# Kernel tuning notes

Measured on AMD Instinct MI355X. Metric: run time of the kernel, lower is better.

## Reference

```python
import jax, jax.numpy as jnp
import numpy as np

B, G, C = 32, 50, 80
IMG = 640
STRIDES = (8, 16, 32)
CENTER_RADIUS = 2.5


def _make_grids():
    xs, ys, ss = [], [], []
    for s in STRIDES:
        n = IMG // s
        yv, xv = np.meshgrid(np.arange(n, dtype=np.float32), np.arange(n, dtype=np.float32), indexing='ij')
        xs.append(xv.reshape(-1)); ys.append(yv.reshape(-1))
        ss.append(np.full(n * n, s, dtype=np.float32))
    return np.concatenate(xs), np.concatenate(ys), np.concatenate(ss)


def setup_inputs():
    xg, yg, sg = _make_grids()
    A = xg.shape[0]  # 8400
    ks = jax.random.split(jax.random.key(0), 5)
    # decoded box predictions near grid centers (cxcywh, pixel units)
    ctr = jnp.stack([jnp.asarray((xg + 0.5) * sg), jnp.asarray((yg + 0.5) * sg)], -1)[None] \
        + jax.random.normal(ks[0], (B, A, 2)) * 8.0
    wh = jnp.exp(jax.random.normal(ks[1], (B, A, 2)) * 0.5) * jnp.asarray(sg)[None, :, None] * 4.0
    pred_output = jnp.concatenate([ctr, wh, jax.random.normal(ks[2], (B, A, 1 + C))], -1)  # [B,A,85]
    obj_preds = jax.random.normal(ks[3], (B, A, 1))
    cls_preds = jax.random.normal(ks[4], (B, A, C))
    # labels [B,G,5] = (class, cx, cy, w, h); first num_gt rows valid, rest zero
    rng = np.random.RandomState(0)
    lab = np.zeros((B, G, 5), np.float32)
    for b in range(B):
        ng = rng.randint(5, G)
        lab[b, :ng, 0] = rng.randint(0, C, ng)
        lab[b, :ng, 1:3] = rng.uniform(40.0, IMG - 40.0, (ng, 2))
        lab[b, :ng, 3:5] = rng.uniform(20.0, 160.0, (ng, 2))
    return {"pred_output": pred_output, "obj_preds": obj_preds, "cls_preds": cls_preds,
            "labels": jnp.asarray(lab), "x_shifts": jnp.asarray(xg),
            "y_shifts": jnp.asarray(yg), "strides": jnp.asarray(sg)}


def _pairwise_iou_cxcywh(a, b):
    # a [G,4], b [A,4] -> [G,A]
    tl = jnp.maximum(a[:, None, :2] - a[:, None, 2:] * 0.5, b[None, :, :2] - b[None, :, 2:] * 0.5)
    br = jnp.minimum(a[:, None, :2] + a[:, None, 2:] * 0.5, b[None, :, :2] + b[None, :, 2:] * 0.5)
    area_a = a[:, 2] * a[:, 3]
    area_b = b[:, 2] * b[:, 3]
    en = jnp.all(tl < br, -1).astype(a.dtype)
    area_i = jnp.prod(br - tl, -1) * en
    return area_i / (area_a[:, None] + area_b[None, :] - area_i + 1e-16)


def _assign_one(gt, gt_valid, boxes, cls_logit, obj_logit, xg, yg, sg):
    # SimOTA assignment for a single image, fully vectorized over [G,A].
    # gt [G,5], gt_valid [G], boxes [A,4], cls_logit [A,C], obj_logit [A,1]
    num_gt = gt.shape[0]
    gt_cls = gt[:, 0].astype(jnp.int32)
    gb = gt[:, 1:5]
    xc = (xg + 0.5) * sg
    yc = (yg + 0.5) * sg
    d_box = jnp.stack([
        xc[None, :] - (gb[:, 0:1] - gb[:, 2:3] * 0.5),
        (gb[:, 0:1] + gb[:, 2:3] * 0.5) - xc[None, :],
        yc[None, :] - (gb[:, 1:2] - gb[:, 3:4] * 0.5),
        (gb[:, 1:2] + gb[:, 3:4] * 0.5) - yc[None, :]], -1)
    in_boxes = (jnp.min(d_box, -1) > 0) & gt_valid[:, None]
    d_ctr = jnp.stack([
        xc[None, :] - (gb[:, 0:1] - CENTER_RADIUS * sg[None, :]),
        (gb[:, 0:1] + CENTER_RADIUS * sg[None, :]) - xc[None, :],
        yc[None, :] - (gb[:, 1:2] - CENTER_RADIUS * sg[None, :]),
        (gb[:, 1:2] + CENTER_RADIUS * sg[None, :]) - yc[None, :]], -1)
    in_ctr = (jnp.min(d_ctr, -1) > 0) & gt_valid[:, None]
    fg0 = jnp.any(in_boxes | in_ctr, 0)           # [A] candidate anchors (fg_mask)
    and_ctr = in_boxes & in_ctr                    # [G,A]
    ious = _pairwise_iou_cxcywh(gb, boxes) * fg0[None, :].astype(boxes.dtype) * gt_valid[:, None].astype(boxes.dtype)
    # pairwise BCE(sqrt(sig(cls)*sig(obj)), one_hot) summed over classes, without [G,A,C]
    logq = 0.5 * (jax.nn.log_sigmoid(cls_logit) + jax.nn.log_sigmoid(obj_logit))  # [A,C]
    q = jnp.clip(jnp.exp(logq), 1e-7, 1.0 - 1e-7)
    s_neg = jnp.sum(jnp.log1p(-q), -1)             # [A] sum_c log(1-q_c)
    q_gt = q[:, gt_cls].T                          # [G,A]
    cls_cost = -jnp.log(q_gt) + jnp.log1p(-q_gt) - s_neg[None, :]
    invalid = (~fg0)[None, :] | (~gt_valid)[:, None]
    cost = cls_cost - 3.0 * jnp.log(ious + 1e-8) + 1e5 * (~and_ctr) + 1e9 * invalid
    # dynamic-k: sum of top-10 ious per gt, truncated, min 1
    dyn_k = jnp.maximum(jnp.sum(jax.lax.top_k(ious, 10)[0], -1).astype(jnp.int32), 1)  # [G]
    ranks = jnp.argsort(jnp.argsort(cost, 1), 1)   # rank of each anchor in ascending cost
    matching = (ranks < dyn_k[:, None]) & gt_valid[:, None]
    # resolve anchors claimed by >1 gt: keep min-cost gt
    best_gt = jnp.argmin(cost, 0)                  # [A]
    onehot_best = jnp.arange(num_gt)[:, None] == best_gt[None, :]
    matching = jnp.where(jnp.sum(matching, 0)[None, :] > 1, onehot_best, matching)
    fg = jnp.any(matching, 0)                      # [A] final fg mask
    matched = jnp.argmax(matching, 0)              # [A] matched gt index
    pred_iou = jnp.sum(matching * ious, 0)         # [A]
    cls_t = jax.nn.one_hot(gt_cls[matched], cls_logit.shape[-1], dtype=boxes.dtype) \
        * (pred_iou * fg.astype(boxes.dtype))[:, None]
    return cls_t, fg, matched


def _forward(pred_output, obj_preds, cls_preds, labels, x_shifts, y_shifts, strides):
    bbox = pred_output[:, :, :4]
    gt_valid = labels.sum(-1) > 0
    cls_t, fg, matched = jax.vmap(_assign_one, in_axes=(0, 0, 0, 0, 0, None, None, None))(
        labels, gt_valid, bbox, cls_preds, obj_preds, x_shifts, y_shifts, strides)
    cls_t = jax.lax.stop_gradient(cls_t)  # get_assignments is @torch.no_grad()
    reg_t = jnp.take_along_axis(labels[:, :, 1:5], matched[:, :, None], axis=1)  # [B,A,4]
    fg_f = fg.astype(pred_output.dtype)
    num_fg = jnp.maximum(jnp.sum(fg_f), 1.0)
    # IoU loss (cxcywh), loss = 1 - iou^2, only on fg anchors
    tl = jnp.maximum(bbox[..., :2] - bbox[..., 2:] * 0.5, reg_t[..., :2] - reg_t[..., 2:] * 0.5)
    br = jnp.minimum(bbox[..., :2] + bbox[..., 2:] * 0.5, reg_t[..., :2] + reg_t[..., 2:] * 0.5)
    en = jnp.all(tl < br, -1).astype(bbox.dtype)
    area_i = jnp.prod(br - tl, -1) * en
    area_u = bbox[..., 2] * bbox[..., 3] + reg_t[..., 2] * reg_t[..., 3] - area_i
    iou = area_i / (area_u + 1e-16)
    loss_iou = jnp.sum((1.0 - iou ** 2) * fg_f) / num_fg
    bce = lambda x, y: jax.nn.softplus(x) - x * y  # BCEWithLogits, reduction='none'
    loss_obj = jnp.sum(bce(obj_preds[..., 0], fg_f)) / num_fg
    loss_cls = jnp.sum(bce(cls_preds, cls_t) * fg_f[..., None]) / num_fg
    return 5.0 * loss_iou + loss_obj + loss_cls


def reference(pred_output, obj_preds, cls_preds, labels, x_shifts, y_shifts, strides):
    return _forward(pred_output, obj_preds, cls_preds, labels, x_shifts, y_shifts, strides)
```

## Files before the change

kernel.cpp:

```cpp
#include <hip/hip_runtime.h>
#include <cstdint>
#include <cstddef>

#define BB 32
#define GG 50
#define CC 80
#define AA 8400
#define PCH (5 + CC)
#define NLB ((BB * AA + 255) / 256)
#define FGBIT 63
#define SENTC 3.3e38f
#define SENTI 0x7fffffff

__device__ __forceinline__ float logsig_fast(float x) {
    float e = __expf(-fabsf(x));
    return fminf(x, 0.f) - __logf(1.f + e);
}
__device__ __forceinline__ float softplusf(float x) {
    return fmaxf(x, 0.f) + log1pf(expf(-fabsf(x)));
}

__device__ __forceinline__ float pair_iou(float px, float py, float pw, float ph,
                                          float gx, float gy, float gw, float gh) {
    float tlx = fmaxf(gx - gw * 0.5f, px - pw * 0.5f);
    float tly = fmaxf(gy - gh * 0.5f, py - ph * 0.5f);
    float brx = fminf(gx + gw * 0.5f, px + pw * 0.5f);
    float bry = fminf(gy + gh * 0.5f, py + ph * 0.5f);
    float en = (tlx < brx && tly < bry) ? 1.f : 0.f;
    float ai = (brx - tlx) * (bry - tly) * en;
    return ai / (gw * gh + pw * ph - ai + 1e-16f);
}
__device__ __forceinline__ float cost_val(float x , float lo ,
                                          float sn , float v ,
                                          bool ac, bool f0, bool valid) {
    float lq = 0.5f * (logsig_fast(x) + lo);
    float q = fminf(fmaxf(__expf(lq), 1e-7f), 1.f - 1e-7f);
    float cst = -__logf(q) + __logf(1.f - q) - sn;
    cst -= 3.0f * __logf(v + 1e-8f);
    cst += 100000.0f * (ac ? 0.f : 1.f);
    cst += 1000000000.0f * ((!f0 || !valid) ? 1.f : 0.f);
    return cst;
}

__global__ __launch_bounds__(256)
void k_precompute(const float* __restrict__ pred, const float* __restrict__ obj,
                  const float* __restrict__ cls,
                  float2* __restrict__ lsn, float* __restrict__ sps,
                  float4* __restrict__ pbox) {
    int t = blockIdx.x * blockDim.x + threadIdx.x;
    int i = t >> 2;
    int sub = t & 3;
    if (i >= BB * AA) return;
    float lo = logsig_fast(obj[i]);
    float K = __expf(0.5f * lo);
    const float4* c4 = (const float4*)(cls + (size_t)i * CC);
    float smax = 0.f, psp = 1.f, p1 = 1.f, p2 = 1.f;
#pragma unroll
    for (int j = 0; j < 5; j++) {
        float4 v = c4[sub + 4 * j];
        float xs4[4] = {v.x, v.y, v.z, v.w};
        float pg = 1.f;
#pragma unroll
        for (int u = 0; u < 4; u++) {
            float x = xs4[u];
            float th = __expf(-0.5f * fabsf(x));
            float t2 = th * th;
            smax += fmaxf(x, 0.f);
            psp *= (1.f + t2);
            float qq = K * (x < 0.f ? th : 1.f) * rsqrtf(1.f + t2);
            qq = fminf(fmaxf(qq, 1e-7f), 1.f - 1e-7f);
            pg *= (1.f - qq);
        }
        if (j < 2) p1 *= pg; else p2 *= pg;
    }
    float sp = smax + __logf(psp);
    float sn = __logf(p1) + __logf(p2);
    sp += __shfl_xor(sp, 1); sn += __shfl_xor(sn, 1);
    sp += __shfl_xor(sp, 2); sn += __shfl_xor(sn, 2);
    float pv = pred[(size_t)i * PCH + sub];
    ((float*)pbox)[(size_t)i * 4 + sub] = pv;
    if (sub == 0) {
        lsn[i] = make_float2(lo, sn);
        sps[i] = sp;
    }
}

__global__ void k_geom(const float* __restrict__ labels, const float* __restrict__ xs,
                       const float* __restrict__ ys, const float* __restrict__ ss,
                       unsigned long long* __restrict__ amask,
                       int* __restrict__ clist, int* __restrict__ ccnt) {
    int b = blockIdx.y;
    int a = blockIdx.x * blockDim.x + threadIdx.x;
    __shared__ float lab[GG * 5];
    __shared__ int lv[GG];
    for (int t = threadIdx.x; t < GG * 5; t += blockDim.x) lab[t] = labels[b * GG * 5 + t];
    __syncthreads();
    if (threadIdx.x < GG) {
        const float* r = lab + threadIdx.x * 5;
        lv[threadIdx.x] = ((r[0] + r[1] + r[2] + r[3] + r[4]) > 0.f) ? 1 : 0;
    }
    __syncthreads();
    if (a >= AA) return;
    float s = ss[a];
    float xc = (xs[a] + 0.5f) * s;
    float yc = (ys[a] + 0.5f) * s;
    unsigned long long m = 0;
    int any = 0;
    for (int g = 0; g < GG; g++) {
        if (!lv[g]) continue;
        const float* r = lab + g * 5;
        float gx = r[1], gy = r[2], gw = r[3], gh = r[4];
        float d1 = xc - (gx - gw * 0.5f);
        float d2 = (gx + gw * 0.5f) - xc;
        float d3 = yc - (gy - gh * 0.5f);
        float d4 = (gy + gh * 0.5f) - yc;
        bool ib = fminf(fminf(d1, d2), fminf(d3, d4)) > 0.f;
        float cr = 2.5f * s;
        float e1 = xc - (gx - cr);
        float e2 = (gx + cr) - xc;
        float e3 = yc - (gy - cr);
        float e4 = (gy + cr) - yc;
        bool ic = fminf(fminf(e1, e2), fminf(e3, e4)) > 0.f;
        if (ib || ic) any = 1;
        if (ib && ic) m |= 1ull << g;
    }
    if (any) m |= 1ull << FGBIT;
    amask[b * AA + a] = m;
    int lane = threadIdx.x & 63;
    unsigned long long act = __ballot(m != 0);
    if (act) {
        int leader = __ffsll(act) - 1;
        int base = 0;
        if (lane == leader) base = atomicAdd(&ccnt[b], __popcll(act));
        base = __shfl(base, leader);
        if (m != 0) {
            int off = __popcll(act & ((1ull << lane) - 1ull));
            clist[b * AA + base + off] = a;
        }
    }
}

__global__ __launch_bounds__(256, 4)
void k_assign(const float4* __restrict__ pbox, const float2* __restrict__ lsn,
              const float* __restrict__ cls,
              const unsigned long long* __restrict__ amask,
              const float* __restrict__ labels,
              const int* __restrict__ clist, const int* __restrict__ ccnt,
              unsigned long long* __restrict__ mmask) {
    int w = blockIdx.x;
    int b = w / GG, g = w % GG;
    const float* r = labels + (size_t)w * 5;
    float gcls = r[0], gx = r[1], gy = r[2], gw = r[3], gh = r[4];
    if (!((gcls + gx + gy + gw + gh) > 0.f)) return;
    int gtc = (int)gcls;
    int tid = threadIdx.x;
    int lane = tid & 63;
    int wv = tid >> 6;
    int cnt = ccnt[b];

    float ivl[10];
    float cvl[10];
    int   cil[10];
#pragma unroll
    for (int t = 0; t < 10; t++) { ivl[t] = 0.f; cvl[t] = SENTC; cil[t] = SENTI; }
    int nac = 0;

    for (int i0 = wv * 64; i0 < cnt; i0 += 256) {
        int i = i0 + lane;
        bool inr = i < cnt;
        int a = clist[b * AA + (inr ? i : (cnt - 1))];
        int ia = b * AA + a;
        unsigned long long am = amask[ia];
        float4 pb = pbox[ia];
        bool f0 = inr && ((am >> FGBIT) & 1ull);
        bool ac = inr && ((am >> g) & 1ull);
        nac += __popcll(__ballot(ac));
        float v = f0 ? pair_iou(pb.x, pb.y, pb.z, pb.w, gx, gy, gw, gh) : 0.f;
        {
            float mv = v;
            while (true) {
                unsigned long long mb = __ballot(mv > ivl[9]);
                if (!mb) break;
                int src = __ffsll(mb) - 1;
                float bv = __shfl(mv, src);
#pragma unroll
                for (int t = 0; t < 10; t++)
                    if (bv > ivl[t]) { float tmp = ivl[t]; ivl[t] = bv; bv = tmp; }
                if (lane == src) mv = -1.f;
            }
        }
        {
            float c = SENTC; int id = SENTI;
            if (ac) {
                float x = cls[(size_t)ia * CC + gtc];
                float2 ls = lsn[ia];
                c = cost_val(x, ls.x, ls.y, v, true, true, true);
                id = a;
            }
            while (true) {
                bool enter = (c < cvl[9]) || (c == cvl[9] && id < cil[9]);
                unsigned long long mb = __ballot(enter);
                if (!mb) break;
                int src = __ffsll(mb) - 1;
                float bc = __shfl(c, src);
                int bi = __shfl(id, src);
#pragma unroll
                for (int t = 0; t < 10; t++) {
                    bool sw = (bc < cvl[t]) || (bc == cvl[t] && bi < cil[t]);
                    if (sw) {
                        float tf = cvl[t]; cvl[t] = bc; bc = tf;
                        int ti = cil[t]; cil[t] = bi; bi = ti;
                    }
                }
                if (lane == src) { c = SENTC; id = SENTI; }
            }
        }
    }

    __shared__ float IV[4][10];
    __shared__ float CV[4][10];
    __shared__ int CI[4][10];
    __shared__ int NAC[4];
    __shared__ int s_k, s_n0;
    __shared__ int sel[10];

    if (lane == 0) {
#pragma unroll
        for (int t = 0; t < 10; t++) { IV[wv][t] = ivl[t]; CV[wv][t] = cvl[t]; CI[wv][t] = cil[t]; }
        NAC[wv] = nac;
    }
    __syncthreads();
    if (tid == 0) {
        int h[4] = {0, 0, 0, 0};
        float ssum = 0.f;
        for (int j = 0; j < 10; j++) {
            float bv = -1.f; int bc = 0;
#pragma unroll
            for (int c2 = 0; c2 < 4; c2++)
                if (h[c2] < 10 && IV[c2][h[c2]] > bv) { bv = IV[c2][h[c2]]; bc = c2; }
            ssum += bv;
            h[bc]++;
        }
        int k = (int)ssum;
        if (k < 1) k = 1;
        s_k = k;
        s_n0 = NAC[0] + NAC[1] + NAC[2] + NAC[3];
    }
    __syncthreads();
    int k = s_k;

    if (s_n0 < k) {
        const int chunk = AA / 4;
        int abase = wv * chunk, aend = abase + chunk;
#pragma unroll
        for (int t = 0; t < 10; t++) { cvl[t] = SENTC; cil[t] = SENTI; }
        for (int a0 = abase; a0 < aend; a0 += 64) {
            int a = a0 + lane;
            bool inr = a < aend;
            int ia = b * AA + (inr ? a : (aend - 1));
            unsigned long long am = amask[ia];
            bool f0 = inr && ((am >> FGBIT) & 1ull);
            bool ac = inr && ((am >> g) & 1ull);
            float v = 0.f;
            if (f0) {
                float4 pb = pbox[ia];
                v = pair_iou(pb.x, pb.y, pb.z, pb.w, gx, gy, gw, gh);
            }
            float c = SENTC; int id = SENTI;
            if (inr) {
                float x = cls[(size_t)ia * CC + gtc];
                float2 ls = lsn[ia];
                c = cost_val(x, ls.x, ls.y, v, ac, f0, true);
                id = a;
            }
            while (true) {
                bool enter = (c < cvl[9]) || (c == cvl[9] && id < cil[9]);
                unsigned long long mb = __ballot(enter);
                if (!mb) break;
                int src = __ffsll(mb) - 1;
                float bc = __shfl(c, src);
                int bi = __shfl(id, src);
#pragma unroll
                for (int t = 0; t < 10; t++) {
                    bool sw = (bc < cvl[t]) || (bc == cvl[t] && bi < cil[t]);
                    if (sw) {
                        float tf = cvl[t]; cvl[t] = bc; bc = tf;
                        int ti = cil[t]; cil[t] = bi; bi = ti;
                    }
                }
                if (lane == src) { c = SENTC; id = SENTI; }
            }
        }
        if (lane == 0) {
#pragma unroll
            for (int t = 0; t < 10; t++) { CV[wv][t] = cvl[t]; CI[wv][t] = cil[t]; }
        }
        __syncthreads();
    }

    if (tid == 0) {
        int h[4] = {0, 0, 0, 0};
        for (int j = 0; j < k; j++) {
            float bv = SENTC; int bix = SENTI; int bc = 0;
#pragma unroll
            for (int c2 = 0; c2 < 4; c2++) {
                if (h[c2] < 10) {
                    float av = CV[c2][h[c2]]; int ax = CI[c2][h[c2]];
                    if (av < bv || (av == bv && ax < bix)) { bv = av; bix = ax; bc = c2; }
                }
            }
            sel[j] = bix;
            h[bc]++;
        }
    }
    __syncthreads();
    if (tid < k) {
        atomicOr(&mmask[(size_t)b * AA + sel[tid]], 1ull << g);
    }
}

__global__ void k_loss(const float4* __restrict__ pbox, const float* __restrict__ obj,
                       const float* __restrict__ cls, const float* __restrict__ labels,
                       const float2* __restrict__ lsn,
                       const unsigned long long* __restrict__ amask,
                       const unsigned long long* __restrict__ mmask,
                       const float* __restrict__ sps, float* __restrict__ partial) {
    int i = blockIdx.x * blockDim.x + threadIdx.x;
    float li = 0.f, lo = 0.f, lc = 0.f, nf = 0.f;
    if (i < BB * AA) {
        int b = i / AA, a = i % AA;
        unsigned long long m = mmask[i];
        int cnt = __popcll(m);
        bool fg = (m != 0);
        int mg = 0;
        float4 pb = pbox[i];
        unsigned long long am = amask[i];
        bool f0 = (am >> FGBIT) & 1ull;
        if (cnt > 1) {
            float2 ls = lsn[i];
            float bv = 3.4e38f;
            for (int g = 0; g < GG; g++) {
                const float* r = labels + (size_t)(b * GG + g) * 5;
                float gcls = r[0], gx = r[1], gy = r[2], gw = r[3], gh = r[4];
                bool valid = (gcls + gx + gy + gw + gh) > 0.f;
                int gtc = (int)gcls;
                float raw = pair_iou(pb.x, pb.y, pb.z, pb.w, gx, gy, gw, gh);
                float v = raw * (f0 ? 1.f : 0.f) * (valid ? 1.f : 0.f);
                float x = cls[(size_t)i * CC + gtc];
                bool ac = (am >> g) & 1ull;
                float cst = cost_val(x, ls.x, ls.y, v, ac, f0, valid);
                if (cst < bv) { bv = cst; mg = g; }
            }
        } else if (cnt == 1) {
            mg = __ffsll((unsigned long long)m) - 1;
        }
        float o = obj[i];
        lo = softplusf(o) - (fg ? o : 0.f);
        if (fg) {
            const float* r = labels + (size_t)(b * GG + mg) * 5;
            float gcls = r[0], gx = r[1], gy = r[2], gw = r[3], gh = r[4];
            bool valid = (gcls + gx + gy + gw + gh) > 0.f;
            int gtc = (int)gcls;
            float piou = pair_iou(pb.x, pb.y, pb.z, pb.w, gx, gy, gw, gh)
                         * (f0 ? 1.f : 0.f) * (valid ? 1.f : 0.f);
            float tlx = fmaxf(pb.x - pb.z * 0.5f, gx - gw * 0.5f);
            float tly = fmaxf(pb.y - pb.w * 0.5f, gy - gh * 0.5f);
            float brx = fminf(pb.x + pb.z * 0.5f, gx + gw * 0.5f);
            float bry = fminf(pb.y + pb.w * 0.5f, gy + gh * 0.5f);
            float en = (tlx < brx && tly < bry) ? 1.f : 0.f;
            float ai = (brx - tlx) * (bry - tly) * en;
            float u = pb.z * pb.w + gw * gh - ai;
            float v2 = ai / (u + 1e-16f);
            li = 1.f - v2 * v2;
            lc = sps[i] - cls[(size_t)i * CC + gtc] * piou;
            nf = 1.f;
        }
    }
    for (int off = 32; off; off >>= 1) {
        li += __shfl_down(li, off);
        lo += __shfl_down(lo, off);
        lc += __shfl_down(lc, off);
        nf += __shfl_down(nf, off);
    }
    __shared__ float red[4][4];
    int wid = threadIdx.x >> 6;
    if ((threadIdx.x & 63) == 0) {
        red[wid][0] = li; red[wid][1] = lo; red[wid][2] = lc; red[wid][3] = nf;
    }
    __syncthreads();
    if (threadIdx.x == 0) {
        float s0 = 0.f, s1 = 0.f, s2 = 0.f, s3 = 0.f;
#pragma unroll
        for (int t = 0; t < 4; t++) {
            s0 += red[t][0]; s1 += red[t][1]; s2 += red[t][2]; s3 += red[t][3];
        }
        float4* pb = (float4*)partial;
        pb[blockIdx.x] = make_float4(s0, s1, s2, s3);
    }
}

__global__ void k_final(const float* __restrict__ partial, float* __restrict__ out) {
    int tid = threadIdx.x;
    float s0 = 0.f, s1 = 0.f, s2 = 0.f, s3 = 0.f;
    const float4* pb = (const float4*)partial;
    for (int i = tid; i < NLB; i += 256) {
        float4 v = pb[i];
        s0 += v.x; s1 += v.y; s2 += v.z; s3 += v.w;
    }
    for (int off = 32; off; off >>= 1) {
        s0 += __shfl_down(s0, off);
        s1 += __shfl_down(s1, off);
        s2 += __shfl_down(s2, off);
        s3 += __shfl_down(s3, off);
    }
    __shared__ float red[4][4];
    int wid = tid >> 6;
    if ((tid & 63) == 0) {
        red[wid][0] = s0; red[wid][1] = s1; red[wid][2] = s2; red[wid][3] = s3;
    }
    __syncthreads();
    if (tid == 0) {
        float li = 0.f, lo = 0.f, lc = 0.f, nf = 0.f;
#pragma unroll
        for (int t = 0; t < 4; t++) {
            li += red[t][0]; lo += red[t][1]; lc += red[t][2]; nf += red[t][3];
        }
        nf = fmaxf(nf, 1.f);
        out[0] = (5.f * li + lo + lc) / nf;
    }
}

extern "C" void kernel_launch(void* const* d_in, const int* in_sizes, int n_in,
                              void* d_out, int out_size, void* d_ws, size_t ws_size,
                              hipStream_t stream) {
    const float* pred = (const float*)d_in[0];
    const float* obj  = (const float*)d_in[1];
    const float* cls  = (const float*)d_in[2];
    const float* lab  = (const float*)d_in[3];
    const float* xs   = (const float*)d_in[4];
    const float* ys   = (const float*)d_in[5];
    const float* ss   = (const float*)d_in[6];
    float* out = (float*)d_out;

    const size_t BA = (size_t)BB * AA;

    float2* lsn  = (float2*)d_ws;
    float*  sps  = (float*)(lsn + BA);
    float4* pbox = (float4*)(sps + BA);
    unsigned long long* amask = (unsigned long long*)(pbox + BA);
    unsigned long long* mmask = amask + BA;
    float* partial = (float*)(mmask + BA);
    int* clist = (int*)(partial + (size_t)NLB * 4);
    int* ccnt  = clist + BA;

    hipMemsetAsync(mmask, 0, BA * sizeof(unsigned long long), stream);
    hipMemsetAsync(ccnt, 0, BB * sizeof(int), stream);

    dim3 blk(256);
    k_precompute<<<dim3((BB * AA * 4 + 255) / 256), blk, 0, stream>>>(pred, obj, cls,
                                                                      lsn, sps, pbox);
    k_geom<<<dim3((AA + 255) / 256, BB), blk, 0, stream>>>(lab, xs, ys, ss, amask,
                                                           clist, ccnt);
    k_assign<<<dim3(BB * GG), blk, 0, stream>>>(pbox, lsn, cls, amask, lab,
                                                clist, ccnt, mmask);
    k_loss<<<dim3(NLB), blk, 0, stream>>>(pbox, obj, cls, lab, lsn, amask,
                                          mmask, sps, partial);
    k_final<<<1, blk, 0, stream>>>(partial, out);
}
```

Baseline: 170.6 us.

## Use per-lane top-10 lists with butterfly merge instead of serialized ballot insertion

The per-GT top-k selection used to keep one wave-wide top-10 list, inserting candidates one lane at a time through a ballot/shuffle loop. Now each lane keeps its own private top-10 lists for IoU and cost. At the end, 10 rounds of xor-shuffle argmax/argmin reductions extract the wave's top 10. This removes the serialized insertion loops when many lanes qualify, at the cost of more registers and a fixed reduction cost.

```diff
diff --git a/kernel.cpp b/kernel.cpp
--- a/kernel.cpp
+++ b/kernel.cpp
@@ -163,56 +163,36 @@
     int   cil[10];
 #pragma unroll
     for (int t = 0; t < 10; t++) { ivl[t] = 0.f; cvl[t] = SENTC; cil[t] = SENTI; }
-    int nac = 0;
-
-    for (int i0 = wv * 64; i0 < cnt; i0 += 256) {
-        int i = i0 + lane;
-        bool inr = i < cnt;
-        int a = clist[b * AA + (inr ? i : (cnt - 1))];
+    int nlc = 0;
+
+    for (int i0 = wv * 64 + lane; i0 < cnt; i0 += 256) {
+        int a = clist[b * AA + i0];
         int ia = b * AA + a;
         unsigned long long am = amask[ia];
         float4 pb = pbox[ia];
-        bool f0 = inr && ((am >> FGBIT) & 1ull);
-        bool ac = inr && ((am >> g) & 1ull);
-        nac += __popcll(__ballot(ac));
+        bool f0 = (am >> FGBIT) & 1ull;
+        bool ac = (am >> g) & 1ull;
+        nlc += ac ? 1 : 0;
         float v = f0 ? pair_iou(pb.x, pb.y, pb.z, pb.w, gx, gy, gw, gh) : 0.f;
-        {
+        if (v > ivl[9]) {
             float mv = v;
-            while (true) {
-                unsigned long long mb = __ballot(mv > ivl[9]);
-                if (!mb) break;
-                int src = __ffsll(mb) - 1;
-                float bv = __shfl(mv, src);
-#pragma unroll
-                for (int t = 0; t < 10; t++)
-                    if (bv > ivl[t]) { float tmp = ivl[t]; ivl[t] = bv; bv = tmp; }
-                if (lane == src) mv = -1.f;
-            }
-        }
-        {
-            float c = SENTC; int id = SENTI;
-            if (ac) {
-                float x = cls[(size_t)ia * CC + gtc];
-                float2 ls = lsn[ia];
-                c = cost_val(x, ls.x, ls.y, v, true, true, true);
-                id = a;
-            }
-            while (true) {
-                bool enter = (c < cvl[9]) || (c == cvl[9] && id < cil[9]);
-                unsigned long long mb = __ballot(enter);
-                if (!mb) break;
-                int src = __ffsll(mb) - 1;
-                float bc = __shfl(c, src);
-                int bi = __shfl(id, src);
+#pragma unroll
+            for (int t = 0; t < 10; t++)
+                if (mv > ivl[t]) { float tmp = ivl[t]; ivl[t] = mv; mv = tmp; }
+        }
+        if (ac) {
+            float2 ls = lsn[ia];
+            float c = cost_val(cls[(size_t)ia * CC + gtc], ls.x, ls.y, v, true, true, true);
+            int id = a;
+            if (c < cvl[9] || (c == cvl[9] && id < cil[9])) {
 #pragma unroll
                 for (int t = 0; t < 10; t++) {
-                    bool sw = (bc < cvl[t]) || (bc == cvl[t] && bi < cil[t]);
+                    bool sw = (c < cvl[t]) || (c == cvl[t] && id < cil[t]);
                     if (sw) {
-                        float tf = cvl[t]; cvl[t] = bc; bc = tf;
-                        int ti = cil[t]; cil[t] = bi; bi = ti;
+                        float tf = cvl[t]; cvl[t] = c; c = tf;
+                        int ti = cil[t]; cil[t] = id; id = ti;
                     }
                 }
-                if (lane == src) { c = SENTC; id = SENTI; }
             }
         }
     }
@@ -224,12 +204,51 @@
     __shared__ int s_k, s_n0;
     __shared__ int sel[10];
 
-    if (lane == 0) {
-#pragma unroll
-        for (int t = 0; t < 10; t++) { IV[wv][t] = ivl[t]; CV[wv][t] = cvl[t]; CI[wv][t] = cil[t]; }
-        NAC[wv] = nac;
-    }
-    __syncthreads();
+    {
+        int s = nlc;
+#pragma unroll
+        for (int off = 1; off < 64; off <<= 1) s += __shfl_xor(s, off);
+        if (lane == 0) NAC[wv] = s;
+    }
+
+    for (int rr = 0; rr < 10; rr++) {
+        float bv = ivl[0];
+        int bl = lane;
+#pragma unroll
+        for (int off = 1; off < 64; off <<= 1) {
+            float ov = __shfl_xor(bv, off);
+            int ol = __shfl_xor(bl, off);
+            if (ov > bv || (ov == bv && ol < bl)) { bv = ov; bl = ol; }
+        }
+        if (lane == 0) IV[wv][rr] = bv;
+        if (lane == bl) {
+#pragma unroll
+            for (int t = 0; t < 9; t++) ivl[t] = ivl[t + 1];
+            ivl[9] = 0.f;
+        }
+    }
+
+    for (int rr = 0; rr < 10; rr++) {
+        float bc = cvl[0];
+        int bi = cil[0];
+        int bl = lane;
+#pragma unroll
+        for (int off = 1; off < 64; off <<= 1) {
+            float oc = __shfl_xor(bc, off);
+            int oi = __shfl_xor(bi, off);
+            int ol = __shfl_xor(bl, off);
+            bool tk = (oc < bc) || (oc == bc && (oi < bi || (oi == bi && ol < bl)));
+            if (tk) { bc = oc; bi = oi; bl = ol; }
+        }
+        if (lane == 0) { CV[wv][rr] = bc; CI[wv][rr] = bi; }
+        if (lane == bl) {
+#pragma unroll
+            for (int t = 0; t < 9; t++) { cvl[t] = cvl[t + 1]; cil[t] = cil[t + 1]; }
+            cvl[9] = SENTC; cil[9] = SENTI;
+        }
+    }
+    __syncthreads();
+
     if (tid == 0) {
         int h[4] = {0, 0, 0, 0};
         float ssum = 0.f;
@@ -250,10 +269,10 @@
     int k = s_k;
 
     if (s_n0 < k) {
+#pragma unroll
+        for (int t = 0; t < 10; t++) { cvl[t] = SENTC; cil[t] = SENTI; }
         const int chunk = AA / 4;
         int abase = wv * chunk, aend = abase + chunk;
-#pragma unroll
-        for (int t = 0; t < 10; t++) { cvl[t] = SENTC; cil[t] = SENTI; }
         for (int a0 = abase; a0 < aend; a0 += 64) {
             int a = a0 + lane;
             bool inr = a < aend;
@@ -273,27 +292,35 @@
                 c = cost_val(x, ls.x, ls.y, v, ac, f0, true);
                 id = a;
             }
-            while (true) {
-                bool enter = (c < cvl[9]) || (c == cvl[9] && id < cil[9]);
-                unsigned long long mb = __ballot(enter);
-                if (!mb) break;
-                int src = __ffsll(mb) - 1;
-                float bc = __shfl(c, src);
-                int bi = __shfl(id, src);
+            if (c < cvl[9] || (c == cvl[9] && id < cil[9])) {
 #pragma unroll
                 for (int t = 0; t < 10; t++) {
-                    bool sw = (bc < cvl[t]) || (bc == cvl[t] && bi < cil[t]);
+                    bool sw = (c < cvl[t]) || (c == cvl[t] && id < cil[t]);
                     if (sw) {
-                        float tf = cvl[t]; cvl[t] = bc; bc = tf;
-                        int ti = cil[t]; cil[t] = bi; bi = ti;
+                        float tf = cvl[t]; cvl[t] = c; c = tf;
+                        int ti = cil[t]; cil[t] = id; id = ti;
                     }
                 }
-                if (lane == src) { c = SENTC; id = SENTI; }
-            }
-        }
-        if (lane == 0) {
-#pragma unroll
-            for (int t = 0; t < 10; t++) { CV[wv][t] = cvl[t]; CI[wv][t] = cil[t]; }
+            }
+        }
+        for (int rr = 0; rr < 10; rr++) {
+            float bc = cvl[0];
+            int bi = cil[0];
+            int bl = lane;
+#pragma unroll
+            for (int off = 1; off < 64; off <<= 1) {
+                float oc = __shfl_xor(bc, off);
+                int oi = __shfl_xor(bi, off);
+                int ol = __shfl_xor(bl, off);
+                bool tk = (oc < bc) || (oc == bc && (oi < bi || (oi == bi && ol < bl)));
+                if (tk) { bc = oc; bi = oi; bl = ol; }
+            }
+            if (lane == 0) { CV[wv][rr] = bc; CI[wv][rr] = bi; }
+            if (lane == bl) {
+#pragma unroll
+                for (int t = 0; t < 9; t++) { cvl[t] = cvl[t + 1]; cil[t] = cil[t + 1]; }
+                cvl[9] = SENTC; cil[9] = SENTI;
+            }
         }
         __syncthreads();
     }
```

Measured after the change: 160.6 us. 5.9% less time.
